# Performance work log

Hardware: AMD Instinct MI355X
Metric: run time of the kernel (lower is better)

## Reference

```python
import jax, jax.numpy as jnp
import numpy as np

D, D_r, G, I = 1024, 64, 2, 2
Ng = D // G  # 512
F = (2 * I + 1) * G  # 10 gathered features per group
BATCH = 4096


def _make_idx():
    # Replicates the torch index construction (modulo-wrapped ring neighbors).
    base = 2 * (np.arange(-I, I + 1).reshape(-1, 1) % Ng)  # (2I+1, 1)
    base = np.concatenate([base, base + 1], axis=1).reshape(-1)  # (2*(2I+1),) == (F,)
    idx = np.stack([(base + 2 * i) % D for i in range(Ng)], axis=0)  # (Ng, F)
    return jnp.asarray(idx, dtype=jnp.int64)


def setup_inputs() -> dict:
    key = jax.random.key(0)
    k1, k2, k3, k4 = jax.random.split(key, 4)
    x = jax.random.normal(k1, (BATCH, D), dtype=jnp.float32)
    # torch.nn.Linear init scale ~ 1/sqrt(fan_in)
    W_in = jax.random.normal(k2, (D_r, F), dtype=jnp.float32) / np.sqrt(F)
    b_in = jax.random.normal(k3, (D_r,), dtype=jnp.float32) / np.sqrt(F)
    W_out = jax.random.normal(k4, (G, D_r), dtype=jnp.float32) / np.sqrt(D_r)
    return {"x": x, "W_in": W_in, "b_in": b_in, "W_out": W_out, "idx": _make_idx()}


def reference(x, W_in, b_in, W_out, idx):
    # gather ring neighbors: [B, Ng, F]
    g = x[..., idx]
    # inner linear + tanh: [B, Ng, D_r]
    h = jnp.tanh(jnp.einsum('bnf,rf->bnr', g, W_in) + b_in)
    # outer linear (no bias): [B, Ng, G] -> reshape to [B, D]
    y = jnp.einsum('bnr,gr->bng', h, W_out).reshape(x.shape)
    return x + y
```

## Files before the change

kernel.cpp:

```cpp
#include <hip/hip_runtime.h>

typedef __fp16 half8    __attribute__((ext_vector_type(8)));
typedef __fp16 half2v   __attribute__((ext_vector_type(2)));
typedef float  float16v __attribute__((ext_vector_type(16)));

#if defined(__has_builtin) && __has_builtin(__builtin_amdgcn_fdot2)
#define DOT2(a, b, c) __builtin_amdgcn_fdot2((a), (b), (c), false)
#else
#define DOT2(a, b, c) ((c) + (float)(a).x * (float)(b).x + (float)(a).y * (float)(b).y)
#endif

__global__ __launch_bounds__(256) void pe_mfma32b(
    const float* __restrict__ x, const float* __restrict__ W_in,
    const float* __restrict__ b_in, const float* __restrict__ W_out,
    float* __restrict__ out, int batch)
{
    __shared__ __align__(16) float sx[4][1056];
    __shared__ __align__(16) float sWin[640];
    __shared__ __align__(16) float sWout[128];
    __shared__ __align__(16) float sb[64];

    const int t    = threadIdx.x;
    const int lane = t & 63;
    const int wv   = t >> 6;
    const int n32  = lane & 31;
    const int g    = lane >> 5;
    const int row0 = 4 * blockIdx.x;
    const int nrows = (batch - row0 >= 4) ? 4 : (batch - row0);

    for (int r = 0; r < nrows; ++r) {
        const float* xr = x + (size_t)(row0 + r) * 1024;
        reinterpret_cast<float4*>(sx[r] + 4)[t] = reinterpret_cast<const float4*>(xr)[t];
        if (t < 4) { sx[r][t] = xr[1020 + t]; sx[r][1028 + t] = xr[t]; }
    }
    if (t < 160)
        reinterpret_cast<float4*>(sWin)[t] = reinterpret_cast<const float4*>(W_in)[t];
    else if (t >= 160 && t < 192)
        reinterpret_cast<float4*>(sWout)[t - 160] = reinterpret_cast<const float4*>(W_out)[t - 160];
    else if (t >= 192 && t < 208)
        reinterpret_cast<float4*>(sb)[t - 192] = reinterpret_cast<const float4*>(b_in)[t - 192];
    __syncthreads();

    half8 Af[2];
    #pragma unroll
    for (int mf = 0; mf < 2; ++mf) {
        const int R = 32 * mf + n32;
        #pragma unroll
        for (int j = 0; j < 8; ++j) {
            const int k = 8 * g + j;
            const float w = (k < 10) ? sWin[R * 10 + k] : (k == 10 ? sb[R] : 0.f);
            Af[mf][j] = (__fp16)w;
        }
    }
    half2v Wp[2][8][2];
    #pragma unroll
    for (int mf = 0; mf < 2; ++mf)
        #pragma unroll
        for (int p = 0; p < 8; ++p) {
            const int R = 32 * mf + ((p & 1) << 1) + 8 * (p >> 1) + 4 * g;
            #pragma unroll
            for (int o = 0; o < 2; ++o)
                Wp[mf][p][o] = __builtin_amdgcn_cvt_pkrtz(sWout[o * 64 + R], sWout[o * 64 + R + 1]);
        }

    const half2v C0 = {(__fp16)0.98931f,     (__fp16)0.98931f};
    const half2v C1 = {(__fp16)-0.26964f,    (__fp16)-0.26964f};
    const half2v C2 = {(__fp16)0.054759f,    (__fp16)0.054759f};
    const half2v C3 = {(__fp16)-0.0057126f,  (__fp16)-0.0057126f};
    const half2v C4 = {(__fp16)0.00022867f,  (__fp16)0.00022867f};
    const half2v HI = {(__fp16)3.0f,  (__fp16)3.0f};
    const half2v LO = {(__fp16)-3.0f, (__fp16)-3.0f};
    const half2v ONE0 = {(__fp16)1.0f, (__fp16)0.0f};
    const half2v ZER0 = {(__fp16)0.0f, (__fp16)0.0f};
    const float16v Zacc = {};

    for (int row = 0; row < nrows; ++row) {
        const float* sxr = sx[row];
        float* orow = out + (size_t)(row0 + row) * 1024;

        half8 Bf[4];
        #pragma unroll
        for (int it = 0; it < 4; ++it) {
            const int n    = (wv * 4 + it) * 32 + n32;
            const int base = 2 * n + 8 * g;
            half2v hp[4];
            #pragma unroll
            for (int p = 0; p < 4; ++p) {
                const float2 q = *reinterpret_cast<const float2*>(sxr + base + 2 * p);
                hp[p] = __builtin_amdgcn_cvt_pkrtz(q.x, q.y);
            }
            if (g) { hp[1] = ONE0; hp[2] = ZER0; hp[3] = ZER0; }
            #pragma unroll
            for (int p = 0; p < 4; ++p) { Bf[it][2 * p] = hp[p].x; Bf[it][2 * p + 1] = hp[p].y; }
        }

        #pragma unroll
        for (int it = 0; it < 4; ++it) {
            float a00 = 0.f, a01 = 0.f, a10 = 0.f, a11 = 0.f;
            #pragma unroll
            for (int mf = 0; mf < 2; ++mf) {
                const float16v D = __builtin_amdgcn_mfma_f32_32x32x16_f16(Af[mf], Bf[it], Zacc, 0, 0, 0);
                #pragma unroll
                for (int p = 0; p < 8; ++p) {
                    half2v zt = __builtin_amdgcn_cvt_pkrtz(D[2 * p], D[2 * p + 1]);
                    zt = __builtin_elementwise_min(__builtin_elementwise_max(zt, LO), HI);
                    const half2v z2 = zt * zt;
                    half2v P = C4;
                    P = P * z2 + C3;
                    P = P * z2 + C2;
                    P = P * z2 + C1;
                    P = P * z2 + C0;
                    const half2v th = zt * P;
                    if (p & 1) {
                        a10 = DOT2(th, Wp[mf][p][0], a10);
                        a11 = DOT2(th, Wp[mf][p][1], a11);
                    } else {
                        a00 = DOT2(th, Wp[mf][p][0], a00);
                        a01 = DOT2(th, Wp[mf][p][1], a01);
                    }
                }
            }
            const float G0 = a00 + a10;
            const float G1 = a01 + a11;

            const half2v pk = __builtin_amdgcn_cvt_pkrtz(G0, G1);
            const int   pi  = __shfl_xor(__builtin_bit_cast(int, pk), 32, 64);
            const half2v sum = pk + __builtin_bit_cast(half2v, pi);

            if (lane < 32) {
                const int n = (wv * 4 + it) * 32 + n32;
                float2 o;
                o.x = (float)Bf[it][4] + (float)sum.x;
                o.y = (float)Bf[it][5] + (float)sum.y;
                *reinterpret_cast<float2*>(orow + 2 * n) = o;
            }
        }
    }
}

extern "C" void kernel_launch(void* const* d_in, const int* in_sizes, int n_in,
                              void* d_out, int out_size, void* d_ws, size_t ws_size,
                              hipStream_t stream) {
    const float* x     = (const float*)d_in[0];
    const float* W_in  = (const float*)d_in[1];
    const float* b_in  = (const float*)d_in[2];
    const float* W_out = (const float*)d_in[3];
    float* out = (float*)d_out;
    const int batch = in_sizes[0] / 1024;
    const int grid  = (batch + 3) / 4;
    pe_mfma32b<<<grid, 256, 0, stream>>>(x, W_in, b_in, W_out, out, batch);
}
```

Before: 104.8 us.

## Stage x as packed fp16 in double-buffered LDS with next-row prefetch

Each block still processes four rows, but now with 512 threads, so each wave handles two 32-group tiles per row instead of four. Each row of x is converted to packed fp16 pairs once and stored in a double-buffered LDS ring with halo entries. The next row is prefetched into registers while the current row is computed. The weights are loaded into registers straight from global memory instead of being staged through LDS. The residual add now happens in fp16 before widening back to fp32, which reduces output precision slightly. The prefetch adds two barriers per row.

```diff
diff --git a/kernel.cpp b/kernel.cpp
--- a/kernel.cpp
+++ b/kernel.cpp
@@ -3,6 +3,7 @@
 typedef __fp16 half8    __attribute__((ext_vector_type(8)));
 typedef __fp16 half2v   __attribute__((ext_vector_type(2)));
 typedef float  float16v __attribute__((ext_vector_type(16)));
+typedef unsigned uint4v __attribute__((ext_vector_type(4)));
 
 #if defined(__has_builtin) && __has_builtin(__builtin_amdgcn_fdot2)
 #define DOT2(a, b, c) __builtin_amdgcn_fdot2((a), (b), (c), false)
@@ -10,15 +11,17 @@
 #define DOT2(a, b, c) ((c) + (float)(a).x * (float)(b).x + (float)(a).y * (float)(b).y)
 #endif
 
-__global__ __launch_bounds__(256) void pe_mfma32b(
+__device__ __forceinline__ unsigned pack2(float a, float b) {
+    const half2v h = __builtin_amdgcn_cvt_pkrtz(a, b);
+    return __builtin_bit_cast(unsigned, h);
+}
+
+__global__ __launch_bounds__(512) void pe_persist(
     const float* __restrict__ x, const float* __restrict__ W_in,
     const float* __restrict__ b_in, const float* __restrict__ W_out,
     float* __restrict__ out, int batch)
 {
-    __shared__ __align__(16) float sx[4][1056];
-    __shared__ __align__(16) float sWin[640];
-    __shared__ __align__(16) float sWout[128];
-    __shared__ __align__(16) float sb[64];
+    __shared__ __align__(16) unsigned sU[2][528];
 
     const int t    = threadIdx.x;
     const int lane = t & 63;
@@ -26,20 +29,6 @@
     const int n32  = lane & 31;
     const int g    = lane >> 5;
     const int row0 = 4 * blockIdx.x;
-    const int nrows = (batch - row0 >= 4) ? 4 : (batch - row0);
-
-    for (int r = 0; r < nrows; ++r) {
-        const float* xr = x + (size_t)(row0 + r) * 1024;
-        reinterpret_cast<float4*>(sx[r] + 4)[t] = reinterpret_cast<const float4*>(xr)[t];
-        if (t < 4) { sx[r][t] = xr[1020 + t]; sx[r][1028 + t] = xr[t]; }
-    }
-    if (t < 160)
-        reinterpret_cast<float4*>(sWin)[t] = reinterpret_cast<const float4*>(W_in)[t];
-    else if (t >= 160 && t < 192)
-        reinterpret_cast<float4*>(sWout)[t - 160] = reinterpret_cast<const float4*>(W_out)[t - 160];
-    else if (t >= 192 && t < 208)
-        reinterpret_cast<float4*>(sb)[t - 192] = reinterpret_cast<const float4*>(b_in)[t - 192];
-    __syncthreads();
 
     half8 Af[2];
     #pragma unroll
@@ -48,7 +37,9 @@
         #pragma unroll
         for (int j = 0; j < 8; ++j) {
             const int k = 8 * g + j;
-            const float w = (k < 10) ? sWin[R * 10 + k] : (k == 10 ? sb[R] : 0.f);
+            float w = 0.f;
+            if (k < 10) w = W_in[R * 10 + k];
+            else if (k == 10) w = b_in[R];
             Af[mf][j] = (__fp16)w;
         }
     }
@@ -60,8 +51,22 @@
             const int R = 32 * mf + ((p & 1) << 1) + 8 * (p >> 1) + 4 * g;
             #pragma unroll
             for (int o = 0; o < 2; ++o)
-                Wp[mf][p][o] = __builtin_amdgcn_cvt_pkrtz(sWout[o * 64 + R], sWout[o * 64 + R + 1]);
+                Wp[mf][p][o] = __builtin_amdgcn_cvt_pkrtz(W_out[o * 64 + R], W_out[o * 64 + R + 1]);
         }
+
+    {
+        const float* xr = x + (size_t)row0 * 1024;
+        const float2 v = reinterpret_cast<const float2*>(xr)[t];
+        const unsigned pk = pack2(v.x, v.y);
+        sU[0][2 + t] = pk;
+        if (t < 2) sU[0][514 + t] = pk;
+        else if (t < 8) sU[0][514 + t] = 0u;
+        if (t >= 2 && t < 4) {
+            const float2 h = *reinterpret_cast<const float2*>(xr + 1020 + 2 * (t - 2));
+            sU[0][t - 2] = pack2(h.x, h.y);
+        }
+    }
+    __syncthreads();
 
     const half2v C0 = {(__fp16)0.98931f,     (__fp16)0.98931f};
     const half2v C1 = {(__fp16)-0.26964f,    (__fp16)-0.26964f};
@@ -70,36 +75,39 @@
     const half2v C4 = {(__fp16)0.00022867f,  (__fp16)0.00022867f};
     const half2v HI = {(__fp16)3.0f,  (__fp16)3.0f};
     const half2v LO = {(__fp16)-3.0f, (__fp16)-3.0f};
-    const half2v ONE0 = {(__fp16)1.0f, (__fp16)0.0f};
-    const half2v ZER0 = {(__fp16)0.0f, (__fp16)0.0f};
     const float16v Zacc = {};
 
-    for (int row = 0; row < nrows; ++row) {
-        const float* sxr = sx[row];
-        float* orow = out + (size_t)(row0 + row) * 1024;
+    for (int r = 0; r < 4; ++r) {
+        if (row0 + r >= batch) break;
+        const int cur = r & 1;
+        const bool pf = (r < 3) && (row0 + r + 1 < batch);
 
-        half8 Bf[4];
-        #pragma unroll
-        for (int it = 0; it < 4; ++it) {
-            const int n    = (wv * 4 + it) * 32 + n32;
-            const int base = 2 * n + 8 * g;
-            half2v hp[4];
-            #pragma unroll
-            for (int p = 0; p < 4; ++p) {
-                const float2 q = *reinterpret_cast<const float2*>(sxr + base + 2 * p);
-                hp[p] = __builtin_amdgcn_cvt_pkrtz(q.x, q.y);
-            }
-            if (g) { hp[1] = ONE0; hp[2] = ZER0; hp[3] = ZER0; }
-            #pragma unroll
-            for (int p = 0; p < 4; ++p) { Bf[it][2 * p] = hp[p].x; Bf[it][2 * p + 1] = hp[p].y; }
+        float2 vmain = {0.f, 0.f}, vhalo = {0.f, 0.f};
+        if (pf) {
+            const float* xn = x + (size_t)(row0 + r + 1) * 1024;
+            vmain = reinterpret_cast<const float2*>(xn)[t];
+            if (t >= 2 && t < 4)
+                vhalo = *reinterpret_cast<const float2*>(xn + 1020 + 2 * (t - 2));
         }
 
+        const unsigned* su = sU[cur];
+        float* orow = out + (size_t)(row0 + r) * 1024;
+
         #pragma unroll
-        for (int it = 0; it < 4; ++it) {
+        for (int it = 0; it < 2; ++it) {
+            const int n  = (wv * 2 + it) * 32 + n32;
+            const int d0 = n + 4 * g;
+            unsigned hp0 = su[d0], hp1 = su[d0 + 1];
+            const unsigned hp2 = su[d0 + 2];
+            unsigned hp2m = hp2, hp3 = su[d0 + 3];
+            if (g) { hp1 = 0x00003C00u; hp2m = 0u; hp3 = 0u; }
+            const uint4v uB = {hp0, hp1, hp2m, hp3};
+            const half8 Bf = __builtin_bit_cast(half8, uB);
+
             float a00 = 0.f, a01 = 0.f, a10 = 0.f, a11 = 0.f;
             #pragma unroll
             for (int mf = 0; mf < 2; ++mf) {
-                const float16v D = __builtin_amdgcn_mfma_f32_32x32x16_f16(Af[mf], Bf[it], Zacc, 0, 0, 0);
+                const float16v D = __builtin_amdgcn_mfma_f32_32x32x16_f16(Af[mf], Bf, Zacc, 0, 0, 0);
                 #pragma unroll
                 for (int p = 0; p < 8; ++p) {
                     half2v zt = __builtin_amdgcn_cvt_pkrtz(D[2 * p], D[2 * p + 1]);
@@ -128,12 +136,24 @@
             const half2v sum = pk + __builtin_bit_cast(half2v, pi);
 
             if (lane < 32) {
-                const int n = (wv * 4 + it) * 32 + n32;
+                const half2v xp = __builtin_bit_cast(half2v, hp2);
+                const half2v o2 = sum + xp;
                 float2 o;
-                o.x = (float)Bf[it][4] + (float)sum.x;
-                o.y = (float)Bf[it][5] + (float)sum.y;
+                o.x = (float)o2.x;
+                o.y = (float)o2.y;
                 *reinterpret_cast<float2*>(orow + 2 * n) = o;
             }
+        }
+
+        if (pf) {
+            __syncthreads();
+            const int nb = cur ^ 1;
+            const unsigned pk = pack2(vmain.x, vmain.y);
+            sU[nb][2 + t] = pk;
+            if (t < 2) sU[nb][514 + t] = pk;
+            else if (t < 8) sU[nb][514 + t] = 0u;
+            if (t >= 2 && t < 4) sU[nb][t - 2] = pack2(vhalo.x, vhalo.y);
+            __syncthreads();
         }
     }
 }
@@ -148,5 +168,5 @@
     float* out = (float*)d_out;
     const int batch = in_sizes[0] / 1024;
     const int grid  = (batch + 3) / 4;
-    pe_mfma32b<<<grid, 256, 0, stream>>>(x, W_in, b_in, W_out, out, batch);
+    pe_persist<<<grid, 512, 0, stream>>>(x, W_in, b_in, W_out, out, batch);
 }
```

New measurement: 102.8 us. Within noise of the previous version (-1.9%).
